# Optimization experiments

Hardware: AMD Instinct MI355X
Metric: run time of the kernel (lower is better)

## Reference

```python
import jax, jax.numpy as jnp
import numpy as np

N = 100000   # nodes
E = 1600000  # edges (avg degree 16)
D = 128      # input_dim = embedding_dim = output_dim
NEG_SLOPE = 0.01  # nn.LeakyReLU default


def setup_inputs() -> dict:
    key = jax.random.key(0)
    k0, k1, k2, k3, k4, k5 = jax.random.split(key, 6)
    x = jax.random.normal(k0, (N, D), jnp.float32)
    edge_index = jax.random.randint(k1, (2, E), 0, N, dtype=jnp.int32)
    batch = jnp.zeros((N,), jnp.int32)
    # GCNConv params (glorot-ish scale)
    W1 = jax.random.normal(k2, (D, D), jnp.float32) * 0.05
    b1 = jax.random.normal(k3, (D,), jnp.float32) * 0.05
    W2 = jax.random.normal(k4, (D, D), jnp.float32) * 0.05
    b2 = jax.random.normal(k5, (D,), jnp.float32) * 0.05
    return {"x": x, "W1": W1, "b1": b1, "W2": W2, "b2": b2,
            "edge_index": edge_index, "batch": batch}


def _gcn_conv(x, W, b, src, dst, deg_isqrt):
    # x' = D^{-1/2} (A + I) D^{-1/2} (x W) + b   (PyG GCNConv defaults)
    h = x @ W                                   # [N, D]
    coef = deg_isqrt[src] * deg_isqrt[dst]      # [E]
    msg = h[src] * coef[:, None]                # [E, D] gather + scale
    out = jax.ops.segment_sum(msg, dst, num_segments=N)  # scatter-add
    out = out + h * (deg_isqrt * deg_isqrt)[:, None]      # self-loop term
    return out + b


def reference(x, W1, b1, W2, b2, edge_index, batch):
    src, dst = edge_index[0], edge_index[1]
    # degree on A + I (self loops), same for both layers
    deg = jax.ops.segment_sum(jnp.ones((E,), x.dtype), dst, num_segments=N) + 1.0
    deg_isqrt = jax.lax.rsqrt(deg)
    h = _gcn_conv(x, W1, b1, src, dst, deg_isqrt)
    h = jax.nn.leaky_relu(h, NEG_SLOPE)
    h = _gcn_conv(h, W2, b2, src, dst, deg_isqrt)
    return jax.nn.leaky_relu(h, NEG_SLOPE)
```

## Files before the change

### kernel.cpp

```cpp
#include <hip/hip_runtime.h>
#include <hip/hip_bf16.h>
#include <stdint.h>

#define NN 100000
#define NE 1600000
#define NR (NE + NN)
#define DD 128
#define NEG 0.01f
#define NB 196
#define EPB 4096
#define NBLK1 391

typedef __attribute__((ext_vector_type(8))) short short8;
typedef __attribute__((ext_vector_type(4))) float floatx4;
typedef __attribute__((ext_vector_type(4))) uint32_t uint32x4;

__device__ __forceinline__ uint16_t f2bf(float f){
  uint32_t i = __float_as_uint(f);
  return (uint16_t)((i + 0x7FFFu + ((i >> 16) & 1u)) >> 16);
}
__device__ __forceinline__ float lrelu(float x){ return fmaxf(x, NEG * x); }

__global__ void k_detect(const uint32_t* __restrict__ xw, int* __restrict__ flag){
  int lane = threadIdx.x;
  uint32_t w = xw[lane];
  uint32_t e = (w >> 7) & 0xFFu;
  int plaus = (e >= 100u && e <= 134u) ? 1 : 0;
  unsigned long long b = __ballot(plaus);
  if (lane == 0) flag[0] = (__popcll(b) >= 48) ? 0 : 1;
}

__global__ __launch_bounds__(256) void k_hist(const int* __restrict__ dst,
                                              int* __restrict__ ghist){
  __shared__ int lh[NB];
  int t = threadIdx.x, b = blockIdx.x;
  if (t < NB) lh[t] = 0;
  __syncthreads();
  #pragma unroll
  for (int i = 0; i < 16; i++){
    int e = b * EPB + i * 256 + t;
    if (e < NE) atomicAdd(&lh[dst[e] >> 9], 1);
  }
  __syncthreads();
  if (t < NB) ghist[t * NBLK1 + b] = lh[t];
}

__global__ __launch_bounds__(512) void k_bscan(int* __restrict__ ghist,
                                               int* __restrict__ btotal){
  __shared__ int sm[512];
  int t = threadIdx.x, bkt = blockIdx.x;
  int v = (t < NBLK1) ? ghist[bkt * NBLK1 + t] : 0;
  sm[t] = v;
  __syncthreads();
  for (int s = 1; s < 512; s <<= 1){
    int add = (t >= s) ? sm[t - s] : 0;
    __syncthreads();
    sm[t] += add;
    __syncthreads();
  }
  if (t < NBLK1) ghist[bkt * NBLK1 + t] = sm[t] - v;
  if (t == 0) btotal[bkt] = sm[511];
}

__global__ __launch_bounds__(256) void k_bscan2(const int* __restrict__ btotal,
                                                int* __restrict__ bucketbase){
  __shared__ int sm[256];
  int t = threadIdx.x;
  int v = (t < NB) ? btotal[t] : 0;
  sm[t] = v;
  __syncthreads();
  for (int s = 1; s < 256; s <<= 1){
    int add = (t >= s) ? sm[t - s] : 0;
    __syncthreads();
    sm[t] += add;
    __syncthreads();
  }
  if (t < NB) bucketbase[t] = sm[t] - v;
  if (t == 0) bucketbase[NB] = sm[255];
}

__global__ __launch_bounds__(256) void k_scatter(const int* __restrict__ src,
                                                 const int* __restrict__ dst,
                                                 const int* __restrict__ ghist,
                                                 const int* __restrict__ bucketbase,
                                                 uint64_t* __restrict__ pairs){
  __shared__ int lcur[NB];
  int t = threadIdx.x, b = blockIdx.x;
  if (t < NB) lcur[t] = bucketbase[t] + ghist[t * NBLK1 + b];
  __syncthreads();
  #pragma unroll
  for (int i = 0; i < 16; i++){
    int e = b * EPB + i * 256 + t;
    if (e < NE){
      int s = src[e], d = dst[e];
      int pos = atomicAdd(&lcur[d >> 9], 1);
      pairs[pos] = ((uint64_t)(uint32_t)d << 32) | (uint32_t)s;
    }
  }
}

__global__ __launch_bounds__(512) void k_bsort(const uint64_t* __restrict__ pairs,
                                               const int* __restrict__ bucketbase,
                                               int2* __restrict__ pairs2,
                                               int* __restrict__ prowstart,
                                               float* __restrict__ dis){
  __shared__ int lcnt[512], lofs[512], sm[512];
  __shared__ float sdn[512];
  int t = threadIdx.x, bkt = blockIdx.x;
  int n0 = bkt << 9;
  int beg = bucketbase[bkt], end = bucketbase[bkt + 1];
  int begS = beg + n0;
  lcnt[t] = 0;
  __syncthreads();
  for (int i = beg + t; i < end; i += 512){
    int d = (int)(pairs[i] >> 32);
    atomicAdd(&lcnt[d - n0], 1);
  }
  __syncthreads();
  int n = n0 + t;
  int inb = (n < NN) ? 1 : 0;
  int v = lcnt[t] + inb;
  sm[t] = v;
  __syncthreads();
  for (int s = 1; s < 512; s <<= 1){
    int add = (t >= s) ? sm[t - s] : 0;
    __syncthreads();
    sm[t] += add;
    __syncthreads();
  }
  int excl = sm[t] - v;
  float dn = rsqrtf((float)(lcnt[t] + 1));
  lofs[t] = excl + 1;
  sdn[t] = dn;
  if (inb){
    prowstart[n] = begS + excl;
    dis[n] = dn;
    pairs2[begS + excl] = make_int2(n, __float_as_int(dn));
  }
  if (bkt == 0 && t == 0) prowstart[NN] = NR;
  __syncthreads();
  for (int i = beg + t; i < end; i += 512){
    uint64_t u = pairs[i];
    int d = (int)(u >> 32);
    int p = atomicAdd(&lofs[d - n0], 1);
    pairs2[begS + p] = make_int2((int)(uint32_t)u, __float_as_int(sdn[d - n0]));
  }
}

__global__ void k_prep2(int2* __restrict__ pairs2, const float* __restrict__ dis){
  int i = blockIdx.x * 256 + threadIdx.x;
  if (i < NR){
    int2 r = pairs2[i];
    r.y = __float_as_int(__int_as_float(r.y) * dis[r.x]);
    pairs2[i] = r;
  }
}

__global__ void k_wb(const void* __restrict__ W1, const void* __restrict__ W2,
                     const void* __restrict__ b1, const void* __restrict__ b2,
                     uint16_t* __restrict__ WT1, uint16_t* __restrict__ WT2,
                     uint16_t* __restrict__ bb, const int* __restrict__ flag){
  int idx = blockIdx.x * 256 + threadIdx.x;
  int f = flag[0];
  if (idx < 16384){
    int c = idx >> 7, k = idx & 127;
    WT1[idx] = f ? f2bf(((const float*)W1)[k * DD + c])
                 : ((const uint16_t*)W1)[k * DD + c];
  } else if (idx < 32768){
    int j = idx - 16384;
    int c = j >> 7, k = j & 127;
    WT2[j] = f ? f2bf(((const float*)W2)[k * DD + c])
               : ((const uint16_t*)W2)[k * DD + c];
  } else if (idx < 33024){
    int j = idx - 32768;
    const void* s = (j < 128) ? b1 : b2;
    int i2 = j & 127;
    bb[j] = f ? f2bf(((const float*)s)[i2]) : ((const uint16_t*)s)[i2];
  }
}

__device__ __forceinline__ short8 ldcvt(const float* __restrict__ p){
  floatx4 u = ((const floatx4*)p)[0], v = ((const floatx4*)p)[1];
  short8 r;
  r[0] = (short)f2bf(u.x); r[1] = (short)f2bf(u.y);
  r[2] = (short)f2bf(u.z); r[3] = (short)f2bf(u.w);
  r[4] = (short)f2bf(v.x); r[5] = (short)f2bf(v.y);
  r[6] = (short)f2bf(v.z); r[7] = (short)f2bf(v.w);
  return r;
}

__global__ __launch_bounds__(256) void k_gemm(const void* __restrict__ X,
                                              const uint16_t* __restrict__ WT,
                                              uint16_t* __restrict__ H,
                                              const int* __restrict__ flag,
                                              int xf32){
  __shared__ uint16_t lwt[128 * 136];
  int t = threadIdx.x;
  const uint32_t* wt32 = (const uint32_t*)WT;
  #pragma unroll
  for (int i = 0; i < 32; i++){
    int uidx = t + 256 * i;
    uint32_t w2 = wt32[uidx];
    int el = uidx * 2;
    int c = el >> 7, k = el & 127;
    *(uint32_t*)&lwt[c * 136 + k] = w2;
  }
  __syncthreads();

  int wave = t >> 6, lane = t & 63;
  int m = lane & 15, q = lane >> 4;
  int rowbase = blockIdx.x * 64 + wave * 16;
  int ar = rowbase + m;
  if (ar >= NN) ar = 0;
  short8 a0, a1, a2, a3;
  if (xf32 && flag[0]){
    const float* xr = (const float*)X + (size_t)ar * DD;
    a0 = ldcvt(xr + q * 8);        a1 = ldcvt(xr + (q + 4) * 8);
    a2 = ldcvt(xr + (q + 8) * 8);  a3 = ldcvt(xr + (q + 12) * 8);
  } else {
    const short8* xrow = (const short8*)((const uint16_t*)X + (size_t)ar * DD);
    a0 = xrow[q]; a1 = xrow[q + 4]; a2 = xrow[q + 8]; a3 = xrow[q + 12];
  }

  #pragma unroll
  for (int nt = 0; nt < 8; nt++){
    int c = nt * 16 + m;
    const uint16_t* bp = &lwt[c * 136 + q * 8];
    floatx4 acc = {0.f, 0.f, 0.f, 0.f};
    acc = __builtin_amdgcn_mfma_f32_16x16x32_bf16(a0, *(const short8*)(bp +  0), acc, 0, 0, 0);
    acc = __builtin_amdgcn_mfma_f32_16x16x32_bf16(a1, *(const short8*)(bp + 32), acc, 0, 0, 0);
    acc = __builtin_amdgcn_mfma_f32_16x16x32_bf16(a2, *(const short8*)(bp + 64), acc, 0, 0, 0);
    acc = __builtin_amdgcn_mfma_f32_16x16x32_bf16(a3, *(const short8*)(bp + 96), acc, 0, 0, 0);
    #pragma unroll
    for (int r = 0; r < 4; r++){
      int row = rowbase + q * 4 + r;
      if (row < NN) H[(size_t)row * DD + c] = f2bf(acc[r]);
    }
  }
}

#define FMA8(VA, CF)                                                     \
  acc[0] = fmaf(__uint_as_float(VA.x << 16),         CF, acc[0]);        \
  acc[1] = fmaf(__uint_as_float(VA.x & 0xffff0000u), CF, acc[1]);        \
  acc[2] = fmaf(__uint_as_float(VA.y << 16),         CF, acc[2]);        \
  acc[3] = fmaf(__uint_as_float(VA.y & 0xffff0000u), CF, acc[3]);        \
  acc[4] = fmaf(__uint_as_float(VA.z << 16),         CF, acc[4]);        \
  acc[5] = fmaf(__uint_as_float(VA.z & 0xffff0000u), CF, acc[5]);        \
  acc[6] = fmaf(__uint_as_float(VA.w << 16),         CF, acc[6]);        \
  acc[7] = fmaf(__uint_as_float(VA.w & 0xffff0000u), CF, acc[7]);

__global__ __launch_bounds__(256) void k_agg(const uint16_t* __restrict__ H,
                                             const int* __restrict__ prow,
                                             const int2* __restrict__ pairs2,
                                             const uint16_t* __restrict__ bias,
                                             void* __restrict__ OUT,
                                             const int* __restrict__ flag,
                                             int is_final){
  __shared__ int2 ebuf[4][2][72];
  int wave = threadIdx.x >> 6, lane = threadIdx.x & 63;
  int grp = lane >> 4, sl = lane & 15;
  if (lane < 8){
    ebuf[wave][0][64 + lane] = make_int2(0, 0);
    ebuf[wave][1][64 + lane] = make_int2(0, 0);
  }
  int n0 = (blockIdx.x * 4 + wave) * 16;
  if (n0 >= NN) return;
  int n1 = min(n0 + 16, NN);
  int pnxt = prow[n0 + 1];
  int beg = prow[n0], cnt = pnxt - beg;
  int2 rec = (lane < cnt) ? pairs2[beg + lane] : make_int2(0, 0);
  int buf = 0;
  int wrf32 = is_final && flag[0];
  uint32x4 bv = ((const uint32x4*)bias)[sl];

  for (int n = n0; n < n1; n++){
    ebuf[wave][buf][lane] = rec;
    int beg2 = 0, cnt2 = 0;
    if (n + 1 < n1){
      int pn2 = prow[n + 2];
      beg2 = pnxt; cnt2 = pn2 - pnxt;
      pnxt = pn2;
    }
    int2 rec2 = (lane < cnt2) ? pairs2[beg2 + lane] : make_int2(0, 0);

    float acc[8] = {0.f,0.f,0.f,0.f,0.f,0.f,0.f,0.f};
    int bcnt = min(cnt, 64);
    int chunks = (bcnt + 3) >> 2;
    int2 ea = ebuf[wave][buf][grp];
    uint32x4 va = *(const uint32x4*)(H + (size_t)ea.x * DD + sl * 8);
    for (int c = 0; c < chunks; c++){
      int2 eb = ebuf[wave][buf][c * 4 + 4 + grp];
      uint32x4 vb = *(const uint32x4*)(H + (size_t)eb.x * DD + sl * 8);
      float cf = __int_as_float(ea.y);
      FMA8(va, cf)
      ea = eb; va = vb;
    }
    for (int done = 64; done < cnt; done += 64){
      int rb = min(cnt - done, 64);
      ebuf[wave][buf][lane] = (lane < rb) ? pairs2[beg + done + lane] : make_int2(0, 0);
      int ch2 = (rb + 3) >> 2;
      ea = ebuf[wave][buf][grp];
      va = *(const uint32x4*)(H + (size_t)ea.x * DD + sl * 8);
      for (int c = 0; c < ch2; c++){
        int2 eb = ebuf[wave][buf][c * 4 + 4 + grp];
        uint32x4 vb = *(const uint32x4*)(H + (size_t)eb.x * DD + sl * 8);
        float cf = __int_as_float(ea.y);
        FMA8(va, cf)
        ea = eb; va = vb;
      }
    }
    #pragma unroll
    for (int j = 0; j < 8; j++){
      acc[j] += __shfl_xor(acc[j], 16, 64);
      acc[j] += __shfl_xor(acc[j], 32, 64);
    }
    float o0 = lrelu(acc[0] + __uint_as_float(bv.x << 16));
    float o1 = lrelu(acc[1] + __uint_as_float(bv.x & 0xffff0000u));
    float o2 = lrelu(acc[2] + __uint_as_float(bv.y << 16));
    float o3 = lrelu(acc[3] + __uint_as_float(bv.y & 0xffff0000u));
    float o4 = lrelu(acc[4] + __uint_as_float(bv.z << 16));
    float o5 = lrelu(acc[5] + __uint_as_float(bv.z & 0xffff0000u));
    float o6 = lrelu(acc[6] + __uint_as_float(bv.w << 16));
    float o7 = lrelu(acc[7] + __uint_as_float(bv.w & 0xffff0000u));
    if (wrf32){
      float* orow = (float*)OUT + (size_t)n * DD + sl * 8;
      if (lane < 16){ floatx4 vv = {o0, o1, o2, o3}; ((floatx4*)orow)[0] = vv; }
      else if (lane < 32){ floatx4 vv = {o4, o5, o6, o7}; ((floatx4*)orow)[1] = vv; }
    } else if (lane < 16){
      uint32x4 pv;
      pv.x = (uint32_t)f2bf(o0) | ((uint32_t)f2bf(o1) << 16);
      pv.y = (uint32_t)f2bf(o2) | ((uint32_t)f2bf(o3) << 16);
      pv.z = (uint32_t)f2bf(o4) | ((uint32_t)f2bf(o5) << 16);
      pv.w = (uint32_t)f2bf(o6) | ((uint32_t)f2bf(o7) << 16);
      *(uint32x4*)((uint16_t*)OUT + (size_t)n * DD + sl * 8) = pv;
    }
    buf ^= 1; rec = rec2; beg = beg2; cnt = cnt2;
  }
}

extern "C" void kernel_launch(void* const* d_in, const int* in_sizes, int n_in,
                              void* d_out, int out_size, void* d_ws, size_t ws_size,
                              hipStream_t stream){
  const void* x  = d_in[0];
  const void* W1 = d_in[1];
  const void* b1 = d_in[2];
  const void* W2 = d_in[3];
  const void* b2 = d_in[4];
  const int* ei   = (const int*)d_in[5];
  const int* esrc = ei;
  const int* edst = ei + NE;

  char* ws = (char*)d_ws;
  float*    dis        = (float*)(ws + 0);
  int*      prow       = (int*)(ws + 512ull * 1024);
  int*      flag       = (int*)(ws + 960ull * 1024);
  uint16_t* WT1        = (uint16_t*)(ws + 964ull * 1024);
  uint16_t* WT2        = (uint16_t*)(ws + 996ull * 1024);
  uint16_t* bb         = (uint16_t*)(ws + 1028ull * 1024);
  int*      ghist      = (int*)(ws + 1032ull * 1024);
  int*      btotal     = (int*)(ws + 1344ull * 1024);
  int*      bucketbase = (int*)(ws + 1348ull * 1024);
  int2*     pairs2     = (int2*)(ws + 2048ull * 1024);
  uint64_t* pairs      = (uint64_t*)(ws + 16384ull * 1024);
  uint16_t* hA         = (uint16_t*)(ws + 16384ull * 1024);
  uint16_t* hB         = (uint16_t*)d_out;

  k_detect<<<1, 64, 0, stream>>>((const uint32_t*)x, flag);
  k_hist  <<<NBLK1, 256, 0, stream>>>(edst, ghist);
  k_bscan <<<NB, 512, 0, stream>>>(ghist, btotal);
  k_bscan2<<<1, 256, 0, stream>>>(btotal, bucketbase);
  k_scatter<<<NBLK1, 256, 0, stream>>>(esrc, edst, ghist, bucketbase, pairs);
  k_bsort <<<NB, 512, 0, stream>>>(pairs, bucketbase, pairs2, prow, dis);
  k_prep2 <<<(NR + 255) / 256, 256, 0, stream>>>(pairs2, dis);
  k_wb    <<<129, 256, 0, stream>>>(W1, W2, b1, b2, WT1, WT2, bb, flag);

  k_gemm<<<(NN + 63) / 64, 256, 0, stream>>>(x, WT1, hA, flag, 1);
  k_agg <<<(NN + 63) / 64, 256, 0, stream>>>(hA, prow, pairs2, bb, hB, flag, 0);
  k_gemm<<<(NN + 63) / 64, 256, 0, stream>>>(hB, WT2, hA, flag, 0);
  k_agg <<<(NN + 63) / 64, 256, 0, stream>>>(hA, prow, pairs2, bb + 128, d_out, flag, 1);
}
```

Baseline: 352.1 us.

## Assign one node per wave in aggregation instead of sixteen nodes

The aggregation kernel now gives each wave a single destination node rather than looping over 16 nodes with double-buffered prefetch of the next node's edge list. The grid grows from about 1.6K blocks to 25K blocks, exposing more parallelism and better load balance across uneven degrees. In exchange it drops the cross-node prefetch of edge records and reloads the bias per wave, which adds per-node latency and launch overhead.

```diff
diff --git a/kernel.cpp b/kernel.cpp
--- a/kernel.cpp
+++ b/kernel.cpp
@@ -256,85 +256,55 @@
                                              void* __restrict__ OUT,
                                              const int* __restrict__ flag,
                                              int is_final){
-  __shared__ int2 ebuf[4][2][72];
+  __shared__ int2 ebuf[4][68];
   int wave = threadIdx.x >> 6, lane = threadIdx.x & 63;
   int grp = lane >> 4, sl = lane & 15;
-  if (lane < 8){
-    ebuf[wave][0][64 + lane] = make_int2(0, 0);
-    ebuf[wave][1][64 + lane] = make_int2(0, 0);
-  }
-  int n0 = (blockIdx.x * 4 + wave) * 16;
-  if (n0 >= NN) return;
-  int n1 = min(n0 + 16, NN);
-  int pnxt = prow[n0 + 1];
-  int beg = prow[n0], cnt = pnxt - beg;
-  int2 rec = (lane < cnt) ? pairs2[beg + lane] : make_int2(0, 0);
-  int buf = 0;
-  int wrf32 = is_final && flag[0];
-  uint32x4 bv = ((const uint32x4*)bias)[sl];
-
-  for (int n = n0; n < n1; n++){
-    ebuf[wave][buf][lane] = rec;
-    int beg2 = 0, cnt2 = 0;
-    if (n + 1 < n1){
-      int pn2 = prow[n + 2];
-      beg2 = pnxt; cnt2 = pn2 - pnxt;
-      pnxt = pn2;
-    }
-    int2 rec2 = (lane < cnt2) ? pairs2[beg2 + lane] : make_int2(0, 0);
-
-    float acc[8] = {0.f,0.f,0.f,0.f,0.f,0.f,0.f,0.f};
-    int bcnt = min(cnt, 64);
-    int chunks = (bcnt + 3) >> 2;
-    int2 ea = ebuf[wave][buf][grp];
+  if (lane < 4) ebuf[wave][64 + lane] = make_int2(0, 0);
+  int n = blockIdx.x * 4 + wave;
+  if (n >= NN) return;
+  int beg = prow[n], end = prow[n + 1];
+
+  float acc[8] = {0.f,0.f,0.f,0.f,0.f,0.f,0.f,0.f};
+  for (int j0 = beg; j0 < end; j0 += 64){
+    int cnt = min(64, end - j0);
+    int2 r = (lane < cnt) ? pairs2[j0 + lane] : make_int2(0, 0);
+    ebuf[wave][lane] = r;
+    int chunks = (cnt + 3) >> 2;
+    int2 ea = ebuf[wave][grp];
     uint32x4 va = *(const uint32x4*)(H + (size_t)ea.x * DD + sl * 8);
     for (int c = 0; c < chunks; c++){
-      int2 eb = ebuf[wave][buf][c * 4 + 4 + grp];
+      int2 eb = ebuf[wave][c * 4 + 4 + grp];
       uint32x4 vb = *(const uint32x4*)(H + (size_t)eb.x * DD + sl * 8);
       float cf = __int_as_float(ea.y);
       FMA8(va, cf)
       ea = eb; va = vb;
     }
-    for (int done = 64; done < cnt; done += 64){
-      int rb = min(cnt - done, 64);
-      ebuf[wave][buf][lane] = (lane < rb) ? pairs2[beg + done + lane] : make_int2(0, 0);
-      int ch2 = (rb + 3) >> 2;
-      ea = ebuf[wave][buf][grp];
-      va = *(const uint32x4*)(H + (size_t)ea.x * DD + sl * 8);
-      for (int c = 0; c < ch2; c++){
-        int2 eb = ebuf[wave][buf][c * 4 + 4 + grp];
-        uint32x4 vb = *(const uint32x4*)(H + (size_t)eb.x * DD + sl * 8);
-        float cf = __int_as_float(ea.y);
-        FMA8(va, cf)
-        ea = eb; va = vb;
-      }
-    }
-    #pragma unroll
-    for (int j = 0; j < 8; j++){
-      acc[j] += __shfl_xor(acc[j], 16, 64);
-      acc[j] += __shfl_xor(acc[j], 32, 64);
-    }
-    float o0 = lrelu(acc[0] + __uint_as_float(bv.x << 16));
-    float o1 = lrelu(acc[1] + __uint_as_float(bv.x & 0xffff0000u));
-    float o2 = lrelu(acc[2] + __uint_as_float(bv.y << 16));
-    float o3 = lrelu(acc[3] + __uint_as_float(bv.y & 0xffff0000u));
-    float o4 = lrelu(acc[4] + __uint_as_float(bv.z << 16));
-    float o5 = lrelu(acc[5] + __uint_as_float(bv.z & 0xffff0000u));
-    float o6 = lrelu(acc[6] + __uint_as_float(bv.w << 16));
-    float o7 = lrelu(acc[7] + __uint_as_float(bv.w & 0xffff0000u));
-    if (wrf32){
-      float* orow = (float*)OUT + (size_t)n * DD + sl * 8;
-      if (lane < 16){ floatx4 vv = {o0, o1, o2, o3}; ((floatx4*)orow)[0] = vv; }
-      else if (lane < 32){ floatx4 vv = {o4, o5, o6, o7}; ((floatx4*)orow)[1] = vv; }
-    } else if (lane < 16){
-      uint32x4 pv;
-      pv.x = (uint32_t)f2bf(o0) | ((uint32_t)f2bf(o1) << 16);
-      pv.y = (uint32_t)f2bf(o2) | ((uint32_t)f2bf(o3) << 16);
-      pv.z = (uint32_t)f2bf(o4) | ((uint32_t)f2bf(o5) << 16);
-      pv.w = (uint32_t)f2bf(o6) | ((uint32_t)f2bf(o7) << 16);
-      *(uint32x4*)((uint16_t*)OUT + (size_t)n * DD + sl * 8) = pv;
-    }
-    buf ^= 1; rec = rec2; beg = beg2; cnt = cnt2;
+  }
+  #pragma unroll
+  for (int j = 0; j < 8; j++){
+    acc[j] += __shfl_xor(acc[j], 16, 64);
+    acc[j] += __shfl_xor(acc[j], 32, 64);
+  }
+  uint32x4 bv = ((const uint32x4*)bias)[sl];
+  float o0 = lrelu(acc[0] + __uint_as_float(bv.x << 16));
+  float o1 = lrelu(acc[1] + __uint_as_float(bv.x & 0xffff0000u));
+  float o2 = lrelu(acc[2] + __uint_as_float(bv.y << 16));
+  float o3 = lrelu(acc[3] + __uint_as_float(bv.y & 0xffff0000u));
+  float o4 = lrelu(acc[4] + __uint_as_float(bv.z << 16));
+  float o5 = lrelu(acc[5] + __uint_as_float(bv.z & 0xffff0000u));
+  float o6 = lrelu(acc[6] + __uint_as_float(bv.w << 16));
+  float o7 = lrelu(acc[7] + __uint_as_float(bv.w & 0xffff0000u));
+  if (is_final && flag[0]){
+    float* orow = (float*)OUT + (size_t)n * DD + sl * 8;
+    if (lane < 16){ floatx4 vv = {o0, o1, o2, o3}; ((floatx4*)orow)[0] = vv; }
+    else if (lane < 32){ floatx4 vv = {o4, o5, o6, o7}; ((floatx4*)orow)[1] = vv; }
+  } else if (lane < 16){
+    uint32x4 pv;
+    pv.x = (uint32_t)f2bf(o0) | ((uint32_t)f2bf(o1) << 16);
+    pv.y = (uint32_t)f2bf(o2) | ((uint32_t)f2bf(o3) << 16);
+    pv.z = (uint32_t)f2bf(o4) | ((uint32_t)f2bf(o5) << 16);
+    pv.w = (uint32_t)f2bf(o6) | ((uint32_t)f2bf(o7) << 16);
+    *(uint32x4*)((uint16_t*)OUT + (size_t)n * DD + sl * 8) = pv;
   }
 }
 
@@ -375,7 +345,7 @@
   k_wb    <<<129, 256, 0, stream>>>(W1, W2, b1, b2, WT1, WT2, bb, flag);
 
   k_gemm<<<(NN + 63) / 64, 256, 0, stream>>>(x, WT1, hA, flag, 1);
-  k_agg <<<(NN + 63) / 64, 256, 0, stream>>>(hA, prow, pairs2, bb, hB, flag, 0);
+  k_agg <<<NN / 4, 256, 0, stream>>>(hA, prow, pairs2, bb, hB, flag, 0);
   k_gemm<<<(NN + 63) / 64, 256, 0, stream>>>(hB, WT2, hA, flag, 0);
-  k_agg <<<(NN + 63) / 64, 256, 0, stream>>>(hA, prow, pairs2, bb + 128, d_out, flag, 1);
-}
+  k_agg <<<NN / 4, 256, 0, stream>>>(hA, prow, pairs2, bb + 128, d_out, flag, 1);
+}
```

Result: faster. 321.4 us (-8.7%).
